# Performance work log

Measured on AMD Instinct MI355X. Metric: run time of the kernel, lower is better.

Reference implementation:

```python
import jax, jax.numpy as jnp
import numpy as np

B, T, C = 2, 192, 512
H, D = 8, 64  # num_heads, head_dim; inner_dim = H*D = C


def setup_inputs() -> dict:
    key = jax.random.key(0)
    k1, k2, k3 = jax.random.split(key, 3)
    x = jax.random.normal(k1, (B, T, C), dtype=jnp.float32)
    W_in = jax.random.normal(k2, (C, 5 * H * D), dtype=jnp.float32) * 0.02
    b_in = jnp.zeros((5 * H * D,), dtype=jnp.float32)
    W_out = jax.random.normal(k3, (H * D, C), dtype=jnp.float32) * 0.02
    b_out = jnp.zeros((C,), dtype=jnp.float32)
    return {"x": x, "W_in": W_in, "b_in": b_in, "W_out": W_out, "b_out": b_out}


def _split_heads(t):
    # (B,T,H*D) -> (B,H,T,D)
    return t.reshape(B, T, H, D).transpose(0, 2, 1, 3)


def reference(x, W_in, b_in, W_out, b_out):
    scale = D ** -0.5
    proj = x @ W_in + b_in  # (B,T,5*H*D)
    q, k1, v1, k2, v2 = jnp.split(proj, 5, axis=-1)
    q = _split_heads(q) * scale
    k1 = _split_heads(k1)
    v1 = _split_heads(v1)
    k2 = _split_heads(k2)
    v2 = _split_heads(v2)
    # trilinear logits: <q_i, k1_j, k2_k> / sqrt(D), computed in fp32
    logits = jnp.einsum('bhid,bhjd,bhkd->bhijk', q, k1, k2,
                        preferred_element_type=jnp.float32)
    # softmax over the joint (j,k) axes
    attn = jax.nn.softmax(logits.reshape(B, H, T, T * T), axis=-1)
    attn = attn.reshape(B, H, T, T, T).astype(x.dtype)
    # out_i[d] = sum_{j,k} attn[i,j,k] * v1_j[d] * v2_k[d]
    out = jnp.einsum('bhijk,bhjd,bhkd->bhid', attn, v1, v2)
    y = out.transpose(0, 2, 1, 3).reshape(B, T, H * D)  # merge heads
    return y @ W_out + b_out
```

## Files before the change

kernel.cpp:

```cpp
#include <hip/hip_runtime.h>
#include <hip/hip_bf16.h>


typedef float  v4f __attribute__((ext_vector_type(4)));
typedef short  v8s __attribute__((ext_vector_type(8)));

__device__ __forceinline__ unsigned short f2bf(float f) {
  unsigned u = __float_as_uint(f);
  u += 0x7fffu + ((u >> 16) & 1u);
  return (unsigned short)(u >> 16);
}
__device__ __forceinline__ float bf2f(unsigned short b) {
  return __uint_as_float(((unsigned)b) << 16);
}
__device__ __forceinline__ unsigned pack_bf16(float lo, float hi) {
  __hip_bfloat162 t = __float22bfloat162_rn(float2{lo, hi});
  union { __hip_bfloat162 b; unsigned u; } cv;
  cv.b = t;
  return cv.u;
}

#if __has_builtin(__builtin_amdgcn_exp2f)
#define EXP2F(x) __builtin_amdgcn_exp2f(x)
#else
#define EXP2F(x) exp2f(x)
#endif

#define MFMA32(a, b, c) __builtin_amdgcn_mfma_f32_16x16x32_bf16((a), (b), (c), 0, 0, 0)

#define QSCALE 0.18033688011112042f


#define XH_OFF   589824
#define XL_OFF   786432
#define WTH_OFF  983040
#define WTL_OFF  2293760
#define WOTH_OFF 3604480
#define WOTL_OFF 3866624
#define OH_OFF   4128768
#define OL_OFF   4325376

__device__ __forceinline__ int v1perm(int t) {
  return (t & ~31) | (((t >> 2) & 3) << 3) | ((t & 3) << 1) | ((t >> 4) & 1);
}

__global__ __launch_bounds__(256) void prep_kernel(
    const float* __restrict__ x, const float* __restrict__ Win,
    const float* __restrict__ Wout, unsigned short* __restrict__ wsh) {
  __shared__ float tile[32 * 65];
  const int bi = blockIdx.x, t = threadIdx.x;
  if (bi < 768) {
    const float* W; unsigned short *Th, *Tl; int R, n0, k0;
    if (bi < 640) {
      W = Win; Th = wsh + WTH_OFF; Tl = wsh + WTL_OFF; R = 2560;
      n0 = (bi % 40) << 6; k0 = (bi / 40) << 5;
    } else {
      const int idx = bi - 640;
      W = Wout; Th = wsh + WOTH_OFF; Tl = wsh + WOTL_OFF; R = 512;
      n0 = (idx & 7) << 6; k0 = (idx >> 3) << 5;
    }
    const int n = t & 63, kq = (t >> 6) * 8;
#pragma unroll
    for (int j = 0; j < 8; ++j)
      tile[(kq + j) * 65 + n] = W[(k0 + kq + j) * R + n0 + n];
    __syncthreads();
    const int n2 = t >> 2, ks = (t & 3) * 8;
    union { uint4 u; unsigned short us[8]; } ph, pl;
#pragma unroll
    for (int j = 0; j < 8; ++j) {
      const float v = tile[(ks + j) * 65 + n2];
      const unsigned short h = f2bf(v);
      ph.us[j] = h;
      pl.us[j] = f2bf(v - bf2f(h));
    }
    *(uint4*)(Th + (n0 + n2) * 512 + k0 + ks) = ph.u;
    *(uint4*)(Tl + (n0 + n2) * 512 + k0 + ks) = pl.u;
  } else {
    const int flat = ((bi - 768) * 256 + t) * 8;
    const v4f v0 = *(const v4f*)(x + flat);
    const v4f v1 = *(const v4f*)(x + flat + 4);
    union { uint4 u; unsigned short us[8]; } ph, pl;
#pragma unroll
    for (int j = 0; j < 4; ++j) {
      unsigned short h = f2bf(v0[j]);
      ph.us[j] = h; pl.us[j] = f2bf(v0[j] - bf2f(h));
      h = f2bf(v1[j]);
      ph.us[4 + j] = h; pl.us[4 + j] = f2bf(v1[j] - bf2f(h));
    }
    *(uint4*)(wsh + XH_OFF + flat) = ph.u;
    *(uint4*)(wsh + XL_OFF + flat) = pl.u;
  }
}

__global__ __launch_bounds__(64) void proj_kernel(
    const unsigned short* __restrict__ wsh, const float* __restrict__ bin,
    float* __restrict__ wsf, unsigned short* __restrict__ wshd) {
  const int lane = threadIdx.x;
  const int c = lane & 15, q = lane >> 4;
  const int bm = blockIdx.x % 12, bn = blockIdx.x / 12;

  const unsigned short* base[8];
  base[0] = wsh + XH_OFF + (bm * 32 + c) * 512 + (q << 3);
  base[1] = base[0] + 16 * 512;
  base[2] = wsh + XL_OFF + (bm * 32 + c) * 512 + (q << 3);
  base[3] = base[2] + 16 * 512;
  base[4] = wsh + WTH_OFF + (bn * 32 + c) * 512 + (q << 3);
  base[5] = base[4] + 16 * 512;
  base[6] = wsh + WTL_OFF + (bn * 32 + c) * 512 + (q << 3);
  base[7] = base[6] + 16 * 512;

  const v4f z = {0.f, 0.f, 0.f, 0.f};
  v4f a00 = z, a01 = z, a10 = z, a11 = z;

  v8s cur[8], nxt[8];
#pragma unroll
  for (int i = 0; i < 8; ++i) cur[i] = *(const v8s*)(base[i]);
#pragma unroll
  for (int i = 0; i < 8; ++i) nxt[i] = *(const v8s*)(base[i] + 32);

#pragma unroll 1
  for (int ks = 0; ks < 16; ++ks) {
    v8s nx2[8];
    if (ks < 14) {
      const int o = (ks + 2) * 32;
#pragma unroll
      for (int i = 0; i < 8; ++i) nx2[i] = *(const v8s*)(base[i] + o);
    }
    a00 = MFMA32(cur[2], cur[4], a00); a00 = MFMA32(cur[0], cur[6], a00); a00 = MFMA32(cur[0], cur[4], a00);
    a01 = MFMA32(cur[2], cur[5], a01); a01 = MFMA32(cur[0], cur[7], a01); a01 = MFMA32(cur[0], cur[5], a01);
    a10 = MFMA32(cur[3], cur[4], a10); a10 = MFMA32(cur[1], cur[6], a10); a10 = MFMA32(cur[1], cur[4], a10);
    a11 = MFMA32(cur[3], cur[5], a11); a11 = MFMA32(cur[1], cur[7], a11); a11 = MFMA32(cur[1], cur[5], a11);
#pragma unroll
    for (int i = 0; i < 8; ++i) { cur[i] = nxt[i]; nxt[i] = nx2[i]; }
  }

  v4f accs[2][2] = {{a00, a01}, {a10, a11}};
#pragma unroll
  for (int mt = 0; mt < 2; ++mt) {
#pragma unroll
    for (int nt = 0; nt < 2; ++nt) {
      const int n = bn * 32 + nt * 16 + c;
      const int which = n >> 9, cc = n & 511, h = cc >> 6, d = cc & 63;
      const float bv = bin[n];
#pragma unroll
      for (int r = 0; r < 4; ++r) {
        const int m = bm * 32 + mt * 16 + (q << 2) + r;
        const int b = (m >= 192) ? 1 : 0;
        const int tt = m - (b ? 192 : 0);
        const int bh = b * 8 + h;
        const float val = accs[mt][nt][r] + bv;
        const int rm = ((bh * 192 + tt) << 6) + d;
        if (which == 0)      wsf[rm] = val * QSCALE;
        else if (which == 1) wshd[rm] = f2bf(val);
        else if (which == 2) wshd[393216 + ((bh << 6) + d) * 192 + v1perm(tt)] = f2bf(val);
        else if (which == 3) wshd[196608 + rm] = f2bf(val);
        else wsf[196608 + ((bh * 192 + tt) * 16 + (d & 15)) * 4 + (d >> 4)] = val;
      }
    }
  }
}

__global__ __launch_bounds__(256, 2) void attn_kernel(
    const float* __restrict__ wsf, const unsigned short* __restrict__ wsh,
    float* __restrict__ accp, float* __restrict__ Sp) {
  __shared__ char smem[58368];
  unsigned short* V1s = (unsigned short*)smem;
  unsigned short* K2s = (unsigned short*)(smem + 25600);

  const int tid  = threadIdx.x;
  const int wv   = tid >> 6;
  const int lane = tid & 63;
  const int c    = lane & 15;
  const int quad = lane >> 4;

  const int bb = blockIdx.x;
  const int kb = bb & 3;
  const int it = (bb >> 2) % 12;
  const int bh = bb / 48;

  const unsigned short* k1g = wsh + bh * 192 * 64;
  const unsigned short* v1g = wsh + 393216 + bh * 64 * 192;
  const unsigned short* k2g = wsh + 196608 + bh * 192 * 64;
  const float*          v2g = wsf + 196608 + bh * 12288;

  for (int idx = tid; idx < 1920; idx += 256) {
    if (idx < 1536) {
      const int r = idx / 24, c8 = (idx % 24) * 8;
      *(uint4*)(V1s + r * 200 + c8) = *(const uint4*)(v1g + r * 192 + c8);
    } else {
      const int j = idx - 1536;
      const int r = j >> 3, c8 = (j & 7) * 8;
      *(uint4*)(K2s + r * 64 + c8) = *(const uint4*)(k2g + (kb * 48 + r) * 64 + c8);
    }
  }

  v8s k1f[12][2];
#pragma unroll
  for (int jt = 0; jt < 12; ++jt) {
    const unsigned short* kp = k1g + ((jt * 16 + c) << 6) + (quad << 3);
    k1f[jt][0] = *(const v8s*)(kp);
    k1f[jt][1] = *(const v8s*)(kp + 32);
  }

  const float* qg = wsf + ((bh * 192 + it * 16 + c) << 6) + (quad << 3);
  float q0[8], q1[8];
  {
    v4f qa = *(const v4f*)(qg), qb = *(const v4f*)(qg + 4);
    v4f qc = *(const v4f*)(qg + 32), qd = *(const v4f*)(qg + 36);
#pragma unroll
    for (int e = 0; e < 4; ++e) {
      q0[e] = qa[e]; q0[4 + e] = qb[e];
      q1[e] = qc[e]; q1[4 + e] = qd[e];
    }
  }
  __syncthreads();

  unsigned* Pw = (unsigned*)(smem + 31744) + wv * 1664;
  const v4f z = {0.f, 0.f, 0.f, 0.f};
  v4f acc[4] = {z, z, z, z};
  v4f oSA = z, oSB = z;
  const short one = (short)0x3F80;
  const v8s ones = {one, one, one, one, one, one, one, one};

  const int kloc0 = wv * 12;
  union U4 { uint4 u4; unsigned short us[8]; };
  union AF { v8s v; unsigned u[4]; };

#pragma unroll 1
  for (int p = 0; p < 6; ++p) {
    const int rA = kloc0 + 2 * p, rB = rA + 1;
    U4 klA, khA, klB, khB;
    klA.u4 = *(const uint4*)(K2s + rA * 64 + (quad << 3));
    khA.u4 = *(const uint4*)(K2s + rA * 64 + (quad << 3) + 32);
    klB.u4 = *(const uint4*)(K2s + rB * 64 + (quad << 3));
    khB.u4 = *(const uint4*)(K2s + rB * 64 + (quad << 3) + 32);
    const v4f v2A = *(const v4f*)(v2g + (((kb * 48 + rA) << 4) + c) * 4);
    const v4f v2B = *(const v4f*)(v2g + (((kb * 48 + rB) << 4) + c) * 4);

    AF af[2][2];
#pragma unroll
    for (int e = 0; e < 4; ++e) {
      af[0][0].u[e] = pack_bf16(q0[2*e] * bf2f(klA.us[2*e]), q0[2*e+1] * bf2f(klA.us[2*e+1]));
      af[0][1].u[e] = pack_bf16(q1[2*e] * bf2f(khA.us[2*e]), q1[2*e+1] * bf2f(khA.us[2*e+1]));
      af[1][0].u[e] = pack_bf16(q0[2*e] * bf2f(klB.us[2*e]), q0[2*e+1] * bf2f(klB.us[2*e+1]));
      af[1][1].u[e] = pack_bf16(q1[2*e] * bf2f(khB.us[2*e]), q1[2*e+1] * bf2f(khB.us[2*e+1]));
    }

    v4f oA[4] = {z, z, z, z}, oB[4] = {z, z, z, z};

#pragma unroll
    for (int h = 0; h < 2; ++h) {
#pragma unroll
      for (int kk = 0; kk < 2; ++kk) {
        v4f C[6];
#pragma unroll
        for (int jj = 0; jj < 6; ++jj) {
          const int jt = h * 6 + jj;
          v4f t0 = MFMA32(af[kk][0].v, k1f[jt][0], z);
          C[jj] = MFMA32(af[kk][1].v, k1f[jt][1], t0);
        }
#pragma unroll
        for (int jj = 0; jj < 6; ++jj)
#pragma unroll
          for (int r = 0; r < 4; ++r) C[jj][r] = EXP2F(C[jj][r]);
#pragma unroll
        for (int m = 0; m < 3; ++m)
#pragma unroll
          for (int r = 0; r < 4; ++r)
            Pw[kk * 832 + ((quad << 2) + r) * 52 + m * 16 + c] =
                pack_bf16(C[2*m][r], C[2*m+1][r]);
      }
#pragma unroll
      for (int m = 0; m < 3; ++m) {
        const v8s apA = *(const v8s*)(Pw + c * 52 + m * 16 + (quad << 2));
        const v8s apB = *(const v8s*)(Pw + 832 + c * 52 + m * 16 + (quad << 2));
        oSA = MFMA32(apA, ones, oSA);
        oSB = MFMA32(apB, ones, oSB);
        const int vcol = (h * 3 + m) * 32 + (quad << 3);
#pragma unroll
        for (int t = 0; t < 4; ++t) {
          const v8s vf = *(const v8s*)(V1s + (c + 16 * t) * 200 + vcol);
          oA[t] = MFMA32(apA, vf, oA[t]);
          oB[t] = MFMA32(apB, vf, oB[t]);
        }
      }
    }
#pragma unroll
    for (int t = 0; t < 4; ++t) acc[t] += oA[t] * v2A[t] + oB[t] * v2B[t];
  }

  __syncthreads();
  float* redA = (float*)smem;
  float* redS = (float*)smem + 4096;

  if (c == 0) {
    float* rs = redS + wv * 16 + (quad << 2);
#pragma unroll
    for (int r = 0; r < 4; ++r) rs[r] = oSA[r] + oSB[r];
  }
#pragma unroll
  for (int r = 0; r < 4; ++r) {
    float* rr = redA + wv * 1024 + (((quad << 2) + r) << 6) + c;
    rr[0] = acc[0][r]; rr[16] = acc[1][r]; rr[32] = acc[2][r]; rr[48] = acc[3][r];
  }
  __syncthreads();

  const int pbase = (bh * 12 + it) * 4 + kb;
  float* ap_out = accp + pbase * 1024;
  for (int idx = tid; idx < 1024; idx += 256)
    ap_out[idx] = redA[idx] + redA[1024 + idx] + redA[2048 + idx] + redA[3072 + idx];
  if (tid < 16)
    Sp[pbase * 16 + tid] = redS[tid] + redS[16 + tid] + redS[32 + tid] + redS[48 + tid];
}

__global__ __launch_bounds__(256) void norm_kernel(
    const float* __restrict__ accp, const float* __restrict__ Sp,
    unsigned short* __restrict__ wsh) {
  const int flat = blockIdx.x * 2048 + threadIdx.x * 8;
  const int m = flat >> 9, cc = flat & 511;
  const int b = (m >= 192) ? 1 : 0;
  const int tt = m - (b ? 192 : 0);
  const int h = cc >> 6, d0 = cc & 63;
  const int bh = b * 8 + h, it = tt >> 4, i = tt & 15;
  const int pb = (bh * 12 + it) * 4;
  const float* ap = accp + pb * 1024 + (i << 6) + d0;
  v4f a0 = *(const v4f*)(ap), a1 = *(const v4f*)(ap + 4);
  float Sv = Sp[pb * 16 + i];
#pragma unroll
  for (int kb = 1; kb < 4; ++kb) {
    a0 += *(const v4f*)(ap + kb * 1024);
    a1 += *(const v4f*)(ap + kb * 1024 + 4);
    Sv += Sp[(pb + kb) * 16 + i];
  }
  const float inv = 1.0f / Sv;
  union { uint4 u; unsigned short us[8]; } ph, pl;
#pragma unroll
  for (int j = 0; j < 4; ++j) {
    float v = a0[j] * inv;
    unsigned short hh = f2bf(v);
    ph.us[j] = hh; pl.us[j] = f2bf(v - bf2f(hh));
    v = a1[j] * inv;
    hh = f2bf(v);
    ph.us[4 + j] = hh; pl.us[4 + j] = f2bf(v - bf2f(hh));
  }
  *(uint4*)(wsh + OH_OFF + flat) = ph.u;
  *(uint4*)(wsh + OL_OFF + flat) = pl.u;
}

__global__ __launch_bounds__(64) void outp_kernel(
    const unsigned short* __restrict__ wsh, const float* __restrict__ bout,
    float* __restrict__ y) {
  const int lane = threadIdx.x;
  const int c = lane & 15, q = lane >> 4;
  const int bm = blockIdx.x % 12, bn = blockIdx.x / 12;

  const unsigned short* base[8];
  base[0] = wsh + OH_OFF + (bm * 32 + c) * 512 + (q << 3);
  base[1] = base[0] + 16 * 512;
  base[2] = wsh + OL_OFF + (bm * 32 + c) * 512 + (q << 3);
  base[3] = base[2] + 16 * 512;
  base[4] = wsh + WOTH_OFF + (bn * 32 + c) * 512 + (q << 3);
  base[5] = base[4] + 16 * 512;
  base[6] = wsh + WOTL_OFF + (bn * 32 + c) * 512 + (q << 3);
  base[7] = base[6] + 16 * 512;

  const v4f z = {0.f, 0.f, 0.f, 0.f};
  v4f a00 = z, a01 = z, a10 = z, a11 = z;

  v8s cur[8], nxt[8];
#pragma unroll
  for (int i = 0; i < 8; ++i) cur[i] = *(const v8s*)(base[i]);
#pragma unroll
  for (int i = 0; i < 8; ++i) nxt[i] = *(const v8s*)(base[i] + 32);

#pragma unroll 1
  for (int ks = 0; ks < 16; ++ks) {
    v8s nx2[8];
    if (ks < 14) {
      const int o = (ks + 2) * 32;
#pragma unroll
      for (int i = 0; i < 8; ++i) nx2[i] = *(const v8s*)(base[i] + o);
    }
    a00 = MFMA32(cur[2], cur[4], a00); a00 = MFMA32(cur[0], cur[6], a00); a00 = MFMA32(cur[0], cur[4], a00);
    a01 = MFMA32(cur[2], cur[5], a01); a01 = MFMA32(cur[0], cur[7], a01); a01 = MFMA32(cur[0], cur[5], a01);
    a10 = MFMA32(cur[3], cur[4], a10); a10 = MFMA32(cur[1], cur[6], a10); a10 = MFMA32(cur[1], cur[4], a10);
    a11 = MFMA32(cur[3], cur[5], a11); a11 = MFMA32(cur[1], cur[7], a11); a11 = MFMA32(cur[1], cur[5], a11);
#pragma unroll
    for (int i = 0; i < 8; ++i) { cur[i] = nxt[i]; nxt[i] = nx2[i]; }
  }

  v4f accs[2][2] = {{a00, a01}, {a10, a11}};
#pragma unroll
  for (int mt = 0; mt < 2; ++mt) {
#pragma unroll
    for (int nt = 0; nt < 2; ++nt) {
      const int n = bn * 32 + nt * 16 + c;
      const float bv = bout[n];
#pragma unroll
      for (int r = 0; r < 4; ++r) {
        const int m = bm * 32 + mt * 16 + (q << 2) + r;
        y[m * 512 + n] = accs[mt][nt][r] + bv;
      }
    }
  }
}

extern "C" void kernel_launch(void* const* d_in, const int* in_sizes, int n_in,
                              void* d_out, int out_size, void* d_ws, size_t ws_size,
                              hipStream_t stream) {
  const float* x    = (const float*)d_in[0];
  const float* Win  = (const float*)d_in[1];
  const float* bin  = (const float*)d_in[2];
  const float* Wout = (const float*)d_in[3];
  const float* bout = (const float*)d_in[4];

  float* wsf = (float*)d_ws;
  unsigned short* wsh = (unsigned short*)(wsf + 1191936);
  float* accp = wsf + 393216;
  float* Sp   = wsf + 1179648;

  prep_kernel<<<dim3(864), 256, 0, stream>>>(x, Win, Wout, wsh);
  proj_kernel<<<dim3(960), 64, 0, stream>>>(wsh, bin, wsf, wsh);
  attn_kernel<<<dim3(768), 256, 0, stream>>>(wsf, wsh, accp, Sp);
  norm_kernel<<<dim3(96), 256, 0, stream>>>(accp, Sp, wsh);
  outp_kernel<<<dim3(192), 64, 0, stream>>>(wsh, bout, (float*)d_out);
}
```

Measured before the change: 146.2 us.

## Load K2/V2 rows from global with register prefetch, drop K2 LDS tile

The K2 shared-memory tile is removed. Each wave now reads its K2 and V2 rows straight from global memory, and the loads for the next iteration are prefetched into registers during the current one. This cuts LDS use from about 58KB to 52KB, and the launch bounds are raised to three blocks per SM to allow more occupancy. The cost is more register pressure under a tighter launch bound, which risks spills, plus uncoalesced global reads in place of the LDS reads.

Result: slower. 209.1 us (+43.1%).

```diff
diff --git a/kernel.cpp b/kernel.cpp
--- a/kernel.cpp
+++ b/kernel.cpp
@@ -160,12 +160,11 @@
   }
 }
 
-__global__ __launch_bounds__(256, 2) void attn_kernel(
+__global__ __launch_bounds__(256, 3) void attn_kernel(
     const float* __restrict__ wsf, const unsigned short* __restrict__ wsh,
     float* __restrict__ accp, float* __restrict__ Sp) {
-  __shared__ char smem[58368];
+  __shared__ char smem[52224];
   unsigned short* V1s = (unsigned short*)smem;
-  unsigned short* K2s = (unsigned short*)(smem + 25600);
 
   const int tid  = threadIdx.x;
   const int wv   = tid >> 6;
@@ -183,15 +182,26 @@
   const unsigned short* k2g = wsh + 196608 + bh * 192 * 64;
   const float*          v2g = wsf + 196608 + bh * 12288;
 
-  for (int idx = tid; idx < 1920; idx += 256) {
-    if (idx < 1536) {
-      const int r = idx / 24, c8 = (idx % 24) * 8;
-      *(uint4*)(V1s + r * 200 + c8) = *(const uint4*)(v1g + r * 192 + c8);
-    } else {
-      const int j = idx - 1536;
-      const int r = j >> 3, c8 = (j & 7) * 8;
-      *(uint4*)(K2s + r * 64 + c8) = *(const uint4*)(k2g + (kb * 48 + r) * 64 + c8);
-    }
+  const int kloc0 = wv * 12;
+
+  const unsigned short* k2r = k2g + ((kb * 48 + kloc0) << 6) + (quad << 3);
+  const float*          v2r = v2g + (((kb * 48 + kloc0) << 4) + c) * 4;
+
+  union U4 { uint4 u4; unsigned short us[8]; };
+  union AF { v8s v; unsigned u[4]; };
+
+  U4 klA, khA, klB, khB;
+  v4f v2A, v2B;
+  klA.u4 = *(const uint4*)(k2r);
+  khA.u4 = *(const uint4*)(k2r + 32);
+  klB.u4 = *(const uint4*)(k2r + 64);
+  khB.u4 = *(const uint4*)(k2r + 96);
+  v2A = *(const v4f*)(v2r);
+  v2B = *(const v4f*)(v2r + 64);
+
+  for (int idx = tid; idx < 1536; idx += 256) {
+    const int r = idx / 24, c8 = (idx % 24) * 8;
+    *(uint4*)(V1s + r * 200 + c8) = *(const uint4*)(v1g + r * 192 + c8);
   }
 
   v8s k1f[12][2];
@@ -215,27 +225,27 @@
   }
   __syncthreads();
 
-  unsigned* Pw = (unsigned*)(smem + 31744) + wv * 1664;
+  unsigned* Pw = (unsigned*)(smem + 25600) + wv * 1664;
   const v4f z = {0.f, 0.f, 0.f, 0.f};
   v4f acc[4] = {z, z, z, z};
   v4f oSA = z, oSB = z;
   const short one = (short)0x3F80;
   const v8s ones = {one, one, one, one, one, one, one, one};
 
-  const int kloc0 = wv * 12;
-  union U4 { uint4 u4; unsigned short us[8]; };
-  union AF { v8s v; unsigned u[4]; };
-
 #pragma unroll 1
   for (int p = 0; p < 6; ++p) {
-    const int rA = kloc0 + 2 * p, rB = rA + 1;
-    U4 klA, khA, klB, khB;
-    klA.u4 = *(const uint4*)(K2s + rA * 64 + (quad << 3));
-    khA.u4 = *(const uint4*)(K2s + rA * 64 + (quad << 3) + 32);
-    klB.u4 = *(const uint4*)(K2s + rB * 64 + (quad << 3));
-    khB.u4 = *(const uint4*)(K2s + rB * 64 + (quad << 3) + 32);
-    const v4f v2A = *(const v4f*)(v2g + (((kb * 48 + rA) << 4) + c) * 4);
-    const v4f v2B = *(const v4f*)(v2g + (((kb * 48 + rB) << 4) + c) * 4);
+    U4 nklA, nkhA, nklB, nkhB;
+    v4f nv2A, nv2B;
+    if (p < 5) {
+      const unsigned short* nk = k2r + (p + 1) * 128;
+      nklA.u4 = *(const uint4*)(nk);
+      nkhA.u4 = *(const uint4*)(nk + 32);
+      nklB.u4 = *(const uint4*)(nk + 64);
+      nkhB.u4 = *(const uint4*)(nk + 96);
+      const float* nv = v2r + (p + 1) * 128;
+      nv2A = *(const v4f*)(nv);
+      nv2B = *(const v4f*)(nv + 64);
+    }
 
     AF af[2][2];
 #pragma unroll
@@ -287,6 +297,9 @@
     }
 #pragma unroll
     for (int t = 0; t < 4; ++t) acc[t] += oA[t] * v2A[t] + oB[t] * v2B[t];
+
+    klA = nklA; khA = nkhA; klB = nklB; khB = nkhB;
+    v2A = nv2A; v2B = nv2B;
   }
 
   __syncthreads();
```
